# Performance work log

Hardware: AMD Instinct MI355X
Metric: run time of the kernel (lower is better)

## Reference

```python
import jax, jax.numpy as jnp
import numpy as np

N_NODES = 10000

def setup_inputs() -> dict:
    key = jax.random.key(0)
    k1, k2, k3, k4, k5 = jax.random.split(key, 5)
    n_edges = 640000
    d_in = 128
    d_out = 128
    x = jax.random.normal(k1, (N_NODES, d_in), dtype=jnp.float32)
    src = jax.random.randint(k2, (n_edges,), 0, N_NODES, dtype=jnp.int32)
    dst = jax.random.randint(k3, (n_edges,), 0, N_NODES, dtype=jnp.int32)
    W = jax.random.normal(k4, (d_in, d_out), dtype=jnp.float32) * (1.0 / np.sqrt(d_in))
    b = jax.random.normal(k5, (d_out,), dtype=jnp.float32) * 0.01
    return {"x": x, "src": src, "dst": dst, "W": W, "b": b}

def reference(x, src, dst, W, b):
    # copy_src + sum reduce: for each edge, send x[src]; each node sums incoming msgs
    msgs = x[src]  # [E, d_in] gather
    h = jax.ops.segment_sum(msgs, dst, num_segments=N_NODES)  # [N, d_in] scatter-add
    # dropout p=0.0 -> identity; linear + relu
    out = jax.nn.relu(h @ W + b)  # [N, d_out]
    return out
```

## Files before the change

kernel.cpp:

```cpp
#include <hip/hip_runtime.h>

#define N_NODES 10000
#define D 128
#define N_EDGES 640000
#define SHARDS 8
#define CSTRIDE 10016
#define BCAP 32

__device__ __forceinline__ unsigned short f2bf(float f) {
  unsigned int u = __float_as_uint(f);
  unsigned int r = (u + 0x7fffu + ((u >> 16) & 1u)) >> 16;
  return (unsigned short)r;
}

__global__ __launch_bounds__(256) void gcn_gemm_kernel(
    const float* __restrict__ x, const float* __restrict__ W,
    unsigned short* __restrict__ xw) {
  __shared__ float Wl[D * D];
  for (int i = threadIdx.x; i < D * D; i += 256) Wl[i] = W[i];
  __syncthreads();

  const int c0 = (threadIdx.x & 31) * 4;
  const int r0 = blockIdx.x * 32 + (threadIdx.x >> 5) * 4;
  if (r0 >= N_NODES) return;

  float4 acc0 = {0,0,0,0}, acc1 = acc0, acc2 = acc0, acc3 = acc0;
  const float* x0 = x + (size_t)r0 * D;

#define GEMM_STEP(J, HC)                                              \
  {                                                                   \
    float4 wv = *(const float4*)&Wl[(k4 + J) * D + c0];               \
    acc0.x = fmaf(hv0.HC, wv.x, acc0.x);                              \
    acc0.y = fmaf(hv0.HC, wv.y, acc0.y);                              \
    acc0.z = fmaf(hv0.HC, wv.z, acc0.z);                              \
    acc0.w = fmaf(hv0.HC, wv.w, acc0.w);                              \
    acc1.x = fmaf(hv1.HC, wv.x, acc1.x);                              \
    acc1.y = fmaf(hv1.HC, wv.y, acc1.y);                              \
    acc1.z = fmaf(hv1.HC, wv.z, acc1.z);                              \
    acc1.w = fmaf(hv1.HC, wv.w, acc1.w);                              \
    acc2.x = fmaf(hv2.HC, wv.x, acc2.x);                              \
    acc2.y = fmaf(hv2.HC, wv.y, acc2.y);                              \
    acc2.z = fmaf(hv2.HC, wv.z, acc2.z);                              \
    acc2.w = fmaf(hv2.HC, wv.w, acc2.w);                              \
    acc3.x = fmaf(hv3.HC, wv.x, acc3.x);                              \
    acc3.y = fmaf(hv3.HC, wv.y, acc3.y);                              \
    acc3.z = fmaf(hv3.HC, wv.z, acc3.z);                              \
    acc3.w = fmaf(hv3.HC, wv.w, acc3.w);                              \
  }

  for (int k4 = 0; k4 < D; k4 += 4) {
    float4 hv0 = *(const float4*)(x0 + 0 * D + k4);
    float4 hv1 = *(const float4*)(x0 + 1 * D + k4);
    float4 hv2 = *(const float4*)(x0 + 2 * D + k4);
    float4 hv3 = *(const float4*)(x0 + 3 * D + k4);
    GEMM_STEP(0, x)
    GEMM_STEP(1, y)
    GEMM_STEP(2, z)
    GEMM_STEP(3, w)
  }
#undef GEMM_STEP

  ushort4 sv;
#define STORE_ROW(R, ACC)                                              \
  sv.x = f2bf(ACC.x); sv.y = f2bf(ACC.y);                              \
  sv.z = f2bf(ACC.z); sv.w = f2bf(ACC.w);                              \
  *(ushort4*)(xw + (size_t)(r0 + R) * D + c0) = sv;
  STORE_ROW(0, acc0)
  STORE_ROW(1, acc1)
  STORE_ROW(2, acc2)
  STORE_ROW(3, acc3)
#undef STORE_ROW
}

__global__ __launch_bounds__(256) void gcn_histfill_kernel(
    const int* __restrict__ src, const int* __restrict__ dst,
    int* __restrict__ counts, unsigned short* __restrict__ srcs_pad) {
  int e = blockIdx.x * 256 + threadIdx.x;
  if (e < N_EDGES) {
    int d = dst[e];
    int sh = blockIdx.x & (SHARDS - 1);
    int r = atomicAdd(&counts[sh * CSTRIDE + d], 1);
    if (r < BCAP)
      srcs_pad[((size_t)d * SHARDS + sh) * BCAP + r] = (unsigned short)src[e];
  }
}

__device__ __forceinline__ void acc8(const unsigned short* __restrict__ xw,
                                     int s, int f, float* a) {
  const uint4 u = *(const uint4*)(xw + (size_t)s * D + f);
  a[0] += __uint_as_float(u.x << 16);
  a[1] += __uint_as_float(u.x & 0xffff0000u);
  a[2] += __uint_as_float(u.y << 16);
  a[3] += __uint_as_float(u.y & 0xffff0000u);
  a[4] += __uint_as_float(u.z << 16);
  a[5] += __uint_as_float(u.z & 0xffff0000u);
  a[6] += __uint_as_float(u.w << 16);
  a[7] += __uint_as_float(u.w & 0xffff0000u);
}

__global__ __launch_bounds__(256) void gcn_gather_kernel(
    const unsigned short* __restrict__ xw, const int* __restrict__ counts,
    const unsigned short* __restrict__ srcs_pad,
    const float* __restrict__ b, float* __restrict__ out) {
  const int node   = blockIdx.x * 16 + (threadIdx.x >> 4);
  const int lane16 = threadIdx.x & 15;
  const int f      = lane16 * 8;
  int c = counts[(lane16 & 7) * CSTRIDE + node];
  const int wbase = (threadIdx.x & 63) & 48;

  float a0[8] = {0,0,0,0,0,0,0,0};
  float a1[8] = {0,0,0,0,0,0,0,0};
  const unsigned short* npad = srcs_pad + (size_t)node * (SHARDS * BCAP);

#pragma unroll
  for (int s = 0; s < SHARDS; ++s) {
    int len = __shfl(c, wbase + s, 64);
    if (len > BCAP) len = BCAP;
    const unsigned short* bp = npad + s * BCAP;
    for (int i = 0; i < len; i += 4) {
      ushort4 s4 = *(const ushort4*)(bp + i);
      acc8(xw, s4.x, f, a0);
      if (i + 1 < len) acc8(xw, s4.y, f, a1);
      if (i + 2 < len) acc8(xw, s4.z, f, a0);
      if (i + 3 < len) acc8(xw, s4.w, f, a1);
    }
  }

  const float4 b0 = *(const float4*)(b + f);
  const float4 b1 = *(const float4*)(b + f + 4);
  float4 o0, o1;
  o0.x = fmaxf(a0[0] + a1[0] + b0.x, 0.f);
  o0.y = fmaxf(a0[1] + a1[1] + b0.y, 0.f);
  o0.z = fmaxf(a0[2] + a1[2] + b0.z, 0.f);
  o0.w = fmaxf(a0[3] + a1[3] + b0.w, 0.f);
  o1.x = fmaxf(a0[4] + a1[4] + b1.x, 0.f);
  o1.y = fmaxf(a0[5] + a1[5] + b1.y, 0.f);
  o1.z = fmaxf(a0[6] + a1[6] + b1.z, 0.f);
  o1.w = fmaxf(a0[7] + a1[7] + b1.w, 0.f);
  *(float4*)(out + (size_t)node * D + f) = o0;
  *(float4*)(out + (size_t)node * D + f + 4) = o1;
}

extern "C" void kernel_launch(void* const* d_in, const int* in_sizes, int n_in,
                              void* d_out, int out_size, void* d_ws, size_t ws_size,
                              hipStream_t stream) {
  const float* x   = (const float*)d_in[0];
  const int*   src = (const int*)d_in[1];
  const int*   dst = (const int*)d_in[2];
  const float* W   = (const float*)d_in[3];
  const float* b   = (const float*)d_in[4];
  float* out = (float*)d_out;

  unsigned short* xw       = (unsigned short*)d_ws;
  int*            counts   = (int*)(xw + (size_t)N_NODES * D);
  unsigned short* srcs_pad = (unsigned short*)(counts + SHARDS * CSTRIDE);

  hipMemsetAsync(counts, 0, SHARDS * CSTRIDE * sizeof(int), stream);

  const int eblocks = (N_EDGES + 255) / 256;
  gcn_gemm_kernel<<<(N_NODES + 31) / 32, 256, 0, stream>>>(x, W, xw);
  gcn_histfill_kernel<<<eblocks, 256, 0, stream>>>(src, dst, counts, srcs_pad);
  gcn_gather_kernel<<<N_NODES / 16, 256, 0, stream>>>(xw, counts, srcs_pad, b, out);
}
```

Before: 137.7 us.

## Fuse GEMM with edge bucketing and remap gather to one wave per node

Merges the GEMM and histogram-fill kernels into one launch, with block ranges split by role, so the two independent stages can overlap and one launch is dropped. W is stored in shared memory as bf16, which halves LDS use and may raise occupancy at the cost of some precision. The gather kernel now gives each node a full 64-lane wave that broadcasts source ids via shuffles and loads one 32-bit word per lane per edge. This trades 16-byte vector loads for narrower, fully coalesced row reads. In the fused kernel, blockIdx & 7 still sets the shard but is now offset by GEMM_BLOCKS, so the shard mapping shifts. Counts are still correct.

```diff
diff --git a/kernel.cpp b/kernel.cpp
--- a/kernel.cpp
+++ b/kernel.cpp
@@ -6,46 +6,69 @@
 #define SHARDS 8
 #define CSTRIDE 10016
 #define BCAP 32
+#define GEMM_BLOCKS 313
+#define FILL_BLOCKS 2500
 
 __device__ __forceinline__ unsigned short f2bf(float f) {
   unsigned int u = __float_as_uint(f);
   unsigned int r = (u + 0x7fffu + ((u >> 16) & 1u)) >> 16;
   return (unsigned short)r;
 }
+__device__ __forceinline__ float bf2f(unsigned short s) {
+  return __uint_as_float((unsigned int)s << 16);
+}
 
-__global__ __launch_bounds__(256) void gcn_gemm_kernel(
+__global__ __launch_bounds__(256) void gcn_gemm_histfill_kernel(
     const float* __restrict__ x, const float* __restrict__ W,
-    unsigned short* __restrict__ xw) {
-  __shared__ float Wl[D * D];
-  for (int i = threadIdx.x; i < D * D; i += 256) Wl[i] = W[i];
+    unsigned short* __restrict__ xw,
+    const int* __restrict__ src, const int* __restrict__ dst,
+    int* __restrict__ counts, unsigned short* __restrict__ srcs_pad) {
+  __shared__ unsigned short Wl[D * D];
+
+  if (blockIdx.x >= GEMM_BLOCKS) {
+    int e = (blockIdx.x - GEMM_BLOCKS) * 256 + threadIdx.x;
+    if (e < N_EDGES) {
+      int d = dst[e];
+      int s = src[e];
+      int sh = blockIdx.x & (SHARDS - 1);
+      int r = atomicAdd(&counts[sh * CSTRIDE + d], 1);
+      if (r < BCAP)
+        srcs_pad[((size_t)d * SHARDS + sh) * BCAP + r] = (unsigned short)s;
+    }
+    return;
+  }
+
+  for (int i = threadIdx.x; i < D * D; i += 256) Wl[i] = f2bf(W[i]);
   __syncthreads();
 
   const int c0 = (threadIdx.x & 31) * 4;
   const int r0 = blockIdx.x * 32 + (threadIdx.x >> 5) * 4;
   if (r0 >= N_NODES) return;
 
-  float4 acc0 = {0,0,0,0}, acc1 = acc0, acc2 = acc0, acc3 = acc0;
+  float4 acc0 = {0, 0, 0, 0}, acc1 = acc0, acc2 = acc0, acc3 = acc0;
   const float* x0 = x + (size_t)r0 * D;
 
 #define GEMM_STEP(J, HC)                                              \
   {                                                                   \
-    float4 wv = *(const float4*)&Wl[(k4 + J) * D + c0];               \
-    acc0.x = fmaf(hv0.HC, wv.x, acc0.x);                              \
-    acc0.y = fmaf(hv0.HC, wv.y, acc0.y);                              \
-    acc0.z = fmaf(hv0.HC, wv.z, acc0.z);                              \
-    acc0.w = fmaf(hv0.HC, wv.w, acc0.w);                              \
-    acc1.x = fmaf(hv1.HC, wv.x, acc1.x);                              \
-    acc1.y = fmaf(hv1.HC, wv.y, acc1.y);                              \
-    acc1.z = fmaf(hv1.HC, wv.z, acc1.z);                              \
-    acc1.w = fmaf(hv1.HC, wv.w, acc1.w);                              \
-    acc2.x = fmaf(hv2.HC, wv.x, acc2.x);                              \
-    acc2.y = fmaf(hv2.HC, wv.y, acc2.y);                              \
-    acc2.z = fmaf(hv2.HC, wv.z, acc2.z);                              \
-    acc2.w = fmaf(hv2.HC, wv.w, acc2.w);                              \
-    acc3.x = fmaf(hv3.HC, wv.x, acc3.x);                              \
-    acc3.y = fmaf(hv3.HC, wv.y, acc3.y);                              \
-    acc3.z = fmaf(hv3.HC, wv.z, acc3.z);                              \
-    acc3.w = fmaf(hv3.HC, wv.w, acc3.w);                              \
+    ushort4 wu = *(const ushort4*)&Wl[(k4 + J) * D + c0];             \
+    float wx = bf2f(wu.x), wy = bf2f(wu.y);                           \
+    float wz = bf2f(wu.z), ww = bf2f(wu.w);                           \
+    acc0.x = fmaf(hv0.HC, wx, acc0.x);                                \
+    acc0.y = fmaf(hv0.HC, wy, acc0.y);                                \
+    acc0.z = fmaf(hv0.HC, wz, acc0.z);                                \
+    acc0.w = fmaf(hv0.HC, ww, acc0.w);                                \
+    acc1.x = fmaf(hv1.HC, wx, acc1.x);                                \
+    acc1.y = fmaf(hv1.HC, wy, acc1.y);                                \
+    acc1.z = fmaf(hv1.HC, wz, acc1.z);                                \
+    acc1.w = fmaf(hv1.HC, ww, acc1.w);                                \
+    acc2.x = fmaf(hv2.HC, wx, acc2.x);                                \
+    acc2.y = fmaf(hv2.HC, wy, acc2.y);                                \
+    acc2.z = fmaf(hv2.HC, wz, acc2.z);                                \
+    acc2.w = fmaf(hv2.HC, ww, acc2.w);                                \
+    acc3.x = fmaf(hv3.HC, wx, acc3.x);                                \
+    acc3.y = fmaf(hv3.HC, wy, acc3.y);                                \
+    acc3.z = fmaf(hv3.HC, wz, acc3.z);                                \
+    acc3.w = fmaf(hv3.HC, ww, acc3.w);                                \
   }
 
   for (int k4 = 0; k4 < D; k4 += 4) {
@@ -72,73 +95,38 @@
 #undef STORE_ROW
 }
 
-__global__ __launch_bounds__(256) void gcn_histfill_kernel(
-    const int* __restrict__ src, const int* __restrict__ dst,
-    int* __restrict__ counts, unsigned short* __restrict__ srcs_pad) {
-  int e = blockIdx.x * 256 + threadIdx.x;
-  if (e < N_EDGES) {
-    int d = dst[e];
-    int sh = blockIdx.x & (SHARDS - 1);
-    int r = atomicAdd(&counts[sh * CSTRIDE + d], 1);
-    if (r < BCAP)
-      srcs_pad[((size_t)d * SHARDS + sh) * BCAP + r] = (unsigned short)src[e];
-  }
-}
-
-__device__ __forceinline__ void acc8(const unsigned short* __restrict__ xw,
-                                     int s, int f, float* a) {
-  const uint4 u = *(const uint4*)(xw + (size_t)s * D + f);
-  a[0] += __uint_as_float(u.x << 16);
-  a[1] += __uint_as_float(u.x & 0xffff0000u);
-  a[2] += __uint_as_float(u.y << 16);
-  a[3] += __uint_as_float(u.y & 0xffff0000u);
-  a[4] += __uint_as_float(u.z << 16);
-  a[5] += __uint_as_float(u.z & 0xffff0000u);
-  a[6] += __uint_as_float(u.w << 16);
-  a[7] += __uint_as_float(u.w & 0xffff0000u);
-}
-
 __global__ __launch_bounds__(256) void gcn_gather_kernel(
     const unsigned short* __restrict__ xw, const int* __restrict__ counts,
     const unsigned short* __restrict__ srcs_pad,
     const float* __restrict__ b, float* __restrict__ out) {
-  const int node   = blockIdx.x * 16 + (threadIdx.x >> 4);
-  const int lane16 = threadIdx.x & 15;
-  const int f      = lane16 * 8;
-  int c = counts[(lane16 & 7) * CSTRIDE + node];
-  const int wbase = (threadIdx.x & 63) & 48;
+  const int node = blockIdx.x * 4 + (threadIdx.x >> 6);
+  const int lane = threadIdx.x & 63;
 
-  float a0[8] = {0,0,0,0,0,0,0,0};
-  float a1[8] = {0,0,0,0,0,0,0,0};
+  int c = 0;
+  if (lane < SHARDS) c = counts[lane * CSTRIDE + node];
+
   const unsigned short* npad = srcs_pad + (size_t)node * (SHARDS * BCAP);
+  const unsigned int* xw32 = (const unsigned int*)xw;
+  float alo = 0.f, ahi = 0.f;
 
 #pragma unroll
   for (int s = 0; s < SHARDS; ++s) {
-    int len = __shfl(c, wbase + s, 64);
+    int len = __shfl(c, s, 64);
     if (len > BCAP) len = BCAP;
-    const unsigned short* bp = npad + s * BCAP;
-    for (int i = 0; i < len; i += 4) {
-      ushort4 s4 = *(const ushort4*)(bp + i);
-      acc8(xw, s4.x, f, a0);
-      if (i + 1 < len) acc8(xw, s4.y, f, a1);
-      if (i + 2 < len) acc8(xw, s4.z, f, a0);
-      if (i + 3 < len) acc8(xw, s4.w, f, a1);
+    int id = npad[s * BCAP + (lane & 31)];
+    for (int j = 0; j < len; ++j) {
+      int sid = __shfl(id, j, 64);
+      unsigned int u = xw32[sid * 64 + lane];
+      alo += __uint_as_float(u << 16);
+      ahi += __uint_as_float(u & 0xffff0000u);
     }
   }
 
-  const float4 b0 = *(const float4*)(b + f);
-  const float4 b1 = *(const float4*)(b + f + 4);
-  float4 o0, o1;
-  o0.x = fmaxf(a0[0] + a1[0] + b0.x, 0.f);
-  o0.y = fmaxf(a0[1] + a1[1] + b0.y, 0.f);
-  o0.z = fmaxf(a0[2] + a1[2] + b0.z, 0.f);
-  o0.w = fmaxf(a0[3] + a1[3] + b0.w, 0.f);
-  o1.x = fmaxf(a0[4] + a1[4] + b1.x, 0.f);
-  o1.y = fmaxf(a0[5] + a1[5] + b1.y, 0.f);
-  o1.z = fmaxf(a0[6] + a1[6] + b1.z, 0.f);
-  o1.w = fmaxf(a0[7] + a1[7] + b1.w, 0.f);
-  *(float4*)(out + (size_t)node * D + f) = o0;
-  *(float4*)(out + (size_t)node * D + f + 4) = o1;
+  const float2 bv = *(const float2*)(b + lane * 2);
+  float2 o;
+  o.x = fmaxf(alo + bv.x, 0.f);
+  o.y = fmaxf(ahi + bv.y, 0.f);
+  *(float2*)(out + (size_t)node * D + lane * 2) = o;
 }
 
 extern "C" void kernel_launch(void* const* d_in, const int* in_sizes, int n_in,
@@ -156,9 +144,7 @@
   unsigned short* srcs_pad = (unsigned short*)(counts + SHARDS * CSTRIDE);
 
   hipMemsetAsync(counts, 0, SHARDS * CSTRIDE * sizeof(int), stream);
-
-  const int eblocks = (N_EDGES + 255) / 256;
-  gcn_gemm_kernel<<<(N_NODES + 31) / 32, 256, 0, stream>>>(x, W, xw);
-  gcn_histfill_kernel<<<eblocks, 256, 0, stream>>>(src, dst, counts, srcs_pad);
-  gcn_gather_kernel<<<N_NODES / 16, 256, 0, stream>>>(xw, counts, srcs_pad, b, out);
+  gcn_gemm_histfill_kernel<<<GEMM_BLOCKS + FILL_BLOCKS, 256, 0, stream>>>(
+      x, W, xw, src, dst, counts, srcs_pad);
+  gcn_gather_kernel<<<N_NODES / 4, 256, 0, stream>>>(xw, counts, srcs_pad, b, out);
 }
```

Result: no change. 139.8 us (+1.6%).
